# Optimization experiments

Hardware: AMD Instinct MI355X
Metric: run time of the kernel (lower is better)

The kernel has to match this reference:

```python
import jax, jax.numpy as jnp
import numpy as np

# config matching init_kwargs
C = 256; G = 16; GC = C // G; K = 3; P = K * K
PAD = 1; STR = 1; DIL = 1; OFFSET_SCALE = 1.0
N, H, W = 8, 64, 64


def setup_inputs() -> dict:
    key = jax.random.key(0)
    ks = jax.random.split(key, 8)
    def rn(k, shape, sc):
        return jax.random.normal(k, shape, jnp.float32) * sc
    return {
        "x": jax.random.normal(ks[0], (N, H, W, C), jnp.float32),
        "dw_w": rn(ks[1], (C, 1, K, K), 0.1),          # depthwise conv weight (OIHW, groups=C)
        "dw_b": jnp.zeros((C,), jnp.float32),
        "ln_g": jnp.ones((C,), jnp.float32),
        "ln_b": jnp.zeros((C,), jnp.float32),
        "off_w": rn(ks[2], (G * P * 2, C), 0.01),      # offset head (small so offsets stay sane)
        "off_b": jnp.zeros((G * P * 2,), jnp.float32),
        "mask_w": rn(ks[3], (G * P, C), 0.01),
        "mask_b": jnp.zeros((G * P,), jnp.float32),
        "in_w": rn(ks[4], (C, C), 0.05),
        "in_b": jnp.zeros((C,), jnp.float32),
        "out_w": rn(ks[5], (C, C), 0.05),
        "out_b": jnp.zeros((C,), jnp.float32),
    }


def _layer_norm(x, g, b, eps=1e-6):
    m = x.mean(-1, keepdims=True)
    v = ((x - m) ** 2).mean(-1, keepdims=True)
    return (x - m) * jax.lax.rsqrt(v + eps) * g + b


def _grid_sample_bilinear(img, grid):
    # img: (B, Cc, Hh, Ww); grid: (B, L, P, 2) normalized to [-1, 1], (x, y) order.
    # Matches torch.grid_sample(mode='bilinear', padding_mode='zeros', align_corners=False).
    B, Cc, Hh, Ww = img.shape
    gx = (grid[..., 0] + 1.0) * (Ww * 0.5) - 0.5
    gy = (grid[..., 1] + 1.0) * (Hh * 0.5) - 0.5
    x0 = jnp.floor(gx); y0 = jnp.floor(gy)
    tx = gx - x0; ty = gy - y0
    img_f = img.reshape(B, Cc, Hh * Ww)
    def corner(xi, yi, w):
        valid = (xi >= 0) & (xi < Ww) & (yi >= 0) & (yi < Hh)
        idx = (jnp.clip(yi, 0, Hh - 1) * Ww + jnp.clip(xi, 0, Ww - 1)).astype(jnp.int32)
        v = jnp.take_along_axis(img_f, idx.reshape(B, 1, -1), axis=2)  # (B, Cc, L*P)
        return v * (w * valid).reshape(B, 1, -1)
    out = (corner(x0, y0, (1 - tx) * (1 - ty)) + corner(x0 + 1, y0, tx * (1 - ty))
           + corner(x0, y0 + 1, (1 - tx) * ty) + corner(x0 + 1, y0 + 1, tx * ty))
    return out.reshape(B, Cc, grid.shape[1], grid.shape[2])  # (B, Cc, L, P)


def _dcnv3_core(x, offset, mask):
    # x: (N,H,W,C) value features; offset: (N,H,W,G*P*2); mask: (N,H,W,G*P)
    xpad = jnp.pad(x, ((0, 0), (PAD, PAD), (PAD, PAD), (0, 0)))
    Hi, Wi = H + 2 * PAD, W + 2 * PAD
    Ho, Wo = H, W
    # reference points (centers of receptive field), normalized by padded size
    start = (DIL * (K - 1)) // 2 + 0.5
    ry = (start + jnp.arange(Ho, dtype=jnp.float32) * STR) / Hi
    rx = (start + jnp.arange(Wo, dtype=jnp.float32) * STR) / Wi
    ref = jnp.stack([jnp.broadcast_to(rx[None, :], (Ho, Wo)),
                     jnp.broadcast_to(ry[:, None], (Ho, Wo))], -1)  # (Ho,Wo,2) (x,y)
    # dilation grid, x-major flattening to match torch meshgrid('ij') ordering
    d = jnp.arange(K, dtype=jnp.float32) * DIL - (DIL * (K - 1)) // 2
    kgrid = jnp.stack([jnp.repeat(d, K) / Wi, jnp.tile(d, K) / Hi], -1)  # (P,2)
    off = offset.reshape(N, Ho, Wo, G, P, 2)
    norm = jnp.array([Wi, Hi], jnp.float32)
    loc = (ref[None, :, :, None, None, :]
           + kgrid[None, None, None, None, :, :] * OFFSET_SCALE
           + off * OFFSET_SCALE / norm)                      # (N,Ho,Wo,G,P,2)
    sg = (2.0 * loc - 1.0).reshape(N, Ho * Wo, G, P, 2)
    sg = sg.transpose(0, 2, 1, 3, 4).reshape(N * G, Ho * Wo, P, 2)
    val = xpad.reshape(N, Hi * Wi, G * GC).transpose(0, 2, 1).reshape(N * G, GC, Hi, Wi)
    samp = _grid_sample_bilinear(val, sg)                    # (N*G, GC, Ho*Wo, P)
    m = mask.reshape(N, Ho * Wo, G, P).transpose(0, 2, 1, 3).reshape(N * G, 1, Ho * Wo, P)
    out = (samp * m).sum(-1)                                 # (N*G, GC, Ho*Wo)
    return out.reshape(N, G * GC, Ho * Wo).transpose(0, 2, 1).reshape(N, Ho, Wo, C)


def reference(x, dw_w, dw_b, ln_g, ln_b, off_w, off_b, mask_w, mask_b, in_w, in_b, out_w, out_b):
    xp = x @ in_w.T + in_b                                   # input_proj (values)
    # depthwise conv -> LN (channels_last) -> exact GELU
    y = jax.lax.conv_general_dilated(
        x.transpose(0, 3, 1, 2), dw_w, (1, 1), ((PAD, PAD), (PAD, PAD)),
        feature_group_count=C, dimension_numbers=('NCHW', 'OIHW', 'NCHW'))
    y = y + dw_b[None, :, None, None]
    x1 = jax.nn.gelu(_layer_norm(y.transpose(0, 2, 3, 1), ln_g, ln_b), approximate=False)
    offset = x1 @ off_w.T + off_b                            # (N,H,W,G*P*2)
    mlogits = (x1 @ mask_w.T + mask_b).reshape(N, H, W, G, P)
    mask = jax.nn.softmax(mlogits, axis=-1).reshape(N, H, W, G * P)
    out = _dcnv3_core(xp, offset, mask)
    return out @ out_w.T + out_b
```

## Files before the change

### kernel.cpp

```cpp
#include <hip/hip_runtime.h>


#define LL 32768
#define CC 256

typedef __bf16 bf16;
typedef __bf16 bf16x4 __attribute__((ext_vector_type(4)));
typedef __bf16 bf16x8 __attribute__((ext_vector_type(8)));
typedef float f32x4v __attribute__((ext_vector_type(4)));

__global__ __launch_bounds__(256) void k_prep(
    const float* __restrict__ in_w, const float* __restrict__ off_w,
    const float* __restrict__ mask_w, const float* __restrict__ out_w,
    const float* __restrict__ dw_w, const float* __restrict__ off_b,
    const float* __restrict__ mask_b,
    bf16* __restrict__ in_h, bf16* __restrict__ in_l,
    bf16* __restrict__ hw_h, bf16* __restrict__ hw_l,
    bf16* __restrict__ out_h, bf16* __restrict__ out_l,
    float* __restrict__ dwT, float* __restrict__ hbias) {
    int idx = blockIdx.x * 256 + threadIdx.x;
    if (idx < 60416) {
        const float* s; bf16 *hi, *lo; int i;
        if (idx < 16384)      { s = in_w;   hi = in_h;          lo = in_l;          i = idx; }
        else if (idx < 34816) { s = off_w;  hi = hw_h;          lo = hw_l;          i = idx - 16384; }
        else if (idx < 44032) { s = mask_w; hi = hw_h + 73728;  lo = hw_l + 73728;  i = idx - 34816; }
        else                  { s = out_w;  hi = out_h;         lo = out_l;         i = idx - 44032; }
        float4 v = *(const float4*)(s + (size_t)i * 4);
        bf16x4 h, l;
        h[0] = (bf16)v.x; l[0] = (bf16)(v.x - (float)h[0]);
        h[1] = (bf16)v.y; l[1] = (bf16)(v.y - (float)h[1]);
        h[2] = (bf16)v.z; l[2] = (bf16)(v.z - (float)h[2]);
        h[3] = (bf16)v.w; l[3] = (bf16)(v.w - (float)h[3]);
        *(bf16x4*)(hi + (size_t)i * 4) = h;
        *(bf16x4*)(lo + (size_t)i * 4) = l;
    } else if (idx < 62720) {
        int e = idx - 60416;
        int c = e & 255, j = e >> 8;
        dwT[j * 256 + c] = dw_w[c * 9 + j];
    } else if (idx < 63152) {
        int e = idx - 62720;
        hbias[e] = (e < 288) ? off_b[e] : mask_b[e - 288];
    }
}

__global__ __launch_bounds__(256) void k_dwln(
    const float* __restrict__ x, const float* __restrict__ dwT,
    const float* __restrict__ dw_b, const float* __restrict__ ln_g,
    const float* __restrict__ ln_b, bf16* __restrict__ x1h) {
    int t = threadIdx.x;
    int q = t >> 6, u = t & 63;
    int l = blockIdx.x * 4 + q;
    int w = l & 63, h = (l >> 6) & 63, n = l >> 12;
    int c0 = u * 4;

    float4 acc = *(const float4*)(dw_b + c0);
#pragma unroll
    for (int kh = 0; kh < 3; ++kh) {
        int hh = h + kh - 1;
        if (hh < 0 || hh >= 64) continue;
#pragma unroll
        for (int kw = 0; kw < 3; ++kw) {
            int ww = w + kw - 1;
            if (ww < 0 || ww >= 64) continue;
            float4 xv = *(const float4*)(x + (size_t)(((n * 64 + hh) * 64) + ww) * CC + c0);
            float4 wv = *(const float4*)(dwT + (kh * 3 + kw) * 256 + c0);
            acc.x += xv.x * wv.x; acc.y += xv.y * wv.y;
            acc.z += xv.z * wv.z; acc.w += xv.w * wv.w;
        }
    }
    float s = acc.x + acc.y + acc.z + acc.w;
    float ss = acc.x * acc.x + acc.y * acc.y + acc.z * acc.z + acc.w * acc.w;
#pragma unroll
    for (int d = 1; d < 64; d <<= 1) {
        s += __shfl_xor(s, d);
        ss += __shfl_xor(ss, d);
    }
    float mean = s * (1.0f / 256.0f);
    float var = ss * (1.0f / 256.0f) - mean * mean;
    float rstd = rsqrtf(var + 1e-6f);
    float4 gv = *(const float4*)(ln_g + c0);
    float4 bv = *(const float4*)(ln_b + c0);
    float xn0 = (acc.x - mean) * rstd * gv.x + bv.x;
    float xn1 = (acc.y - mean) * rstd * gv.y + bv.y;
    float xn2 = (acc.z - mean) * rstd * gv.z + bv.z;
    float xn3 = (acc.w - mean) * rstd * gv.w + bv.w;
    bf16x4 oh;
    oh[0] = (bf16)(0.5f * xn0 * (1.0f + erff(xn0 * 0.70710678118654752f)));
    oh[1] = (bf16)(0.5f * xn1 * (1.0f + erff(xn1 * 0.70710678118654752f)));
    oh[2] = (bf16)(0.5f * xn2 * (1.0f + erff(xn2 * 0.70710678118654752f)));
    oh[3] = (bf16)(0.5f * xn3 * (1.0f + erff(xn3 * 0.70710678118654752f)));
    *(bf16x4*)(x1h + (size_t)l * CC + c0) = oh;
}

template <bool AF32, bool OBF16>
__global__ __launch_bounds__(256) void k_gemm(
    const float* __restrict__ A32, const bf16* __restrict__ Abf,
    const bf16* __restrict__ Wh, const bf16* __restrict__ Wl,
    const float* __restrict__ bias, float* __restrict__ C32,
    bf16* __restrict__ Cbf, int Nout) {
    int mb = blockIdx.x * 128, nb = blockIdx.y * 128;
    int t = threadIdx.x, wave = t >> 6, lane = t & 63;
    int wm = wave & 1, wn = wave >> 1;
    int fm = lane & 15, fq = lane >> 4;

    __shared__ bf16 sA[128][32];
    __shared__ bf16 sWh[128][32];
    __shared__ bf16 sWl[128][32];

    f32x4v acc[4][4];
#pragma unroll
    for (int i = 0; i < 4; ++i)
#pragma unroll
        for (int j = 0; j < 4; ++j) acc[i][j] = (f32x4v){0.f, 0.f, 0.f, 0.f};

    int r = t >> 1;
    int cb = (t & 1) * 16;

    for (int kc = 0; kc < 256; kc += 32) {
        if (AF32) {
            const float* src = A32 + (size_t)(mb + r) * CC + kc + cb;
#pragma unroll
            for (int j = 0; j < 2; ++j) {
                float4 v0 = *(const float4*)(src + j * 8);
                float4 v1 = *(const float4*)(src + j * 8 + 4);
                bf16x8 hh;
                hh[0] = (bf16)v0.x; hh[1] = (bf16)v0.y;
                hh[2] = (bf16)v0.z; hh[3] = (bf16)v0.w;
                hh[4] = (bf16)v1.x; hh[5] = (bf16)v1.y;
                hh[6] = (bf16)v1.z; hh[7] = (bf16)v1.w;
                *(bf16x8*)&sA[r][cb + j * 8] = hh;
            }
        } else {
            const bf16* srcA = Abf + (size_t)(mb + r) * CC + kc + cb;
            *(uint4*)&sA[r][cb]     = *(const uint4*)srcA;
            *(uint4*)&sA[r][cb + 8] = *(const uint4*)(srcA + 8);
        }
        int wng = nb + r;
        if (wng < Nout) {
            const bf16* swH = Wh + (size_t)wng * CC + kc + cb;
            const bf16* swL = Wl + (size_t)wng * CC + kc + cb;
            *(uint4*)&sWh[r][cb]     = *(const uint4*)swH;
            *(uint4*)&sWh[r][cb + 8] = *(const uint4*)(swH + 8);
            *(uint4*)&sWl[r][cb]     = *(const uint4*)swL;
            *(uint4*)&sWl[r][cb + 8] = *(const uint4*)(swL + 8);
        } else {
            uint4 z = {0, 0, 0, 0};
            *(uint4*)&sWh[r][cb] = z; *(uint4*)&sWh[r][cb + 8] = z;
            *(uint4*)&sWl[r][cb] = z; *(uint4*)&sWl[r][cb + 8] = z;
        }
        __syncthreads();

        bf16x8 af[4], bfh[4], bfl[4];
#pragma unroll
        for (int i = 0; i < 4; ++i)
            af[i] = *(const bf16x8*)&sA[wm * 64 + i * 16 + fm][fq * 8];
#pragma unroll
        for (int j = 0; j < 4; ++j) {
            int br = wn * 64 + j * 16 + fm;
            bfh[j] = *(const bf16x8*)&sWh[br][fq * 8];
            bfl[j] = *(const bf16x8*)&sWl[br][fq * 8];
        }
#pragma unroll
        for (int i = 0; i < 4; ++i)
#pragma unroll
            for (int j = 0; j < 4; ++j) {
                acc[i][j] = __builtin_amdgcn_mfma_f32_16x16x32_bf16(
                    af[i], bfh[j], acc[i][j], 0, 0, 0);
                acc[i][j] = __builtin_amdgcn_mfma_f32_16x16x32_bf16(
                    af[i], bfl[j], acc[i][j], 0, 0, 0);
            }
        __syncthreads();
    }

#pragma unroll
    for (int j = 0; j < 4; ++j) {
        int n_g = nb + wn * 64 + j * 16 + fm;
        if (n_g >= Nout) continue;
        float bv = bias[n_g];
#pragma unroll
        for (int i = 0; i < 4; ++i) {
            int m_g = mb + wm * 64 + i * 16 + fq * 4;
#pragma unroll
            for (int rg = 0; rg < 4; ++rg) {
                float o = acc[i][j][rg] + bv;
                if (OBF16)
                    Cbf[(size_t)(m_g + rg) * Nout + n_g] = (bf16)o;
                else
                    C32[(size_t)(m_g + rg) * Nout + n_g] = o;
            }
        }
    }
}

__global__ __launch_bounds__(256) void k_gather(
    const bf16* __restrict__ xp, const float* __restrict__ head,
    bf16* __restrict__ rows) {
    int t = threadIdx.x;
    int q = t >> 5, u = t & 31;
    int l = blockIdx.x * 8 + q;
    int w = l & 63, h = (l >> 6) & 63, n = l >> 12;

    __shared__ float offs[8][288];
    __shared__ float ms[8][144];
    for (int j = u; j < 288; j += 32) offs[q][j] = head[(size_t)l * 432 + j];
    for (int j = u; j < 144; j += 32) ms[q][j] = head[(size_t)l * 432 + 288 + j];
    __syncthreads();

    if (u < 16) {
        int g = u;
        float mx = -1e30f;
#pragma unroll
        for (int p = 0; p < 9; ++p) mx = fmaxf(mx, ms[q][g * 9 + p]);
        float s = 0.f, e[9];
#pragma unroll
        for (int p = 0; p < 9; ++p) { e[p] = expf(ms[q][g * 9 + p] - mx); s += e[p]; }
        float inv = 1.0f / s;
#pragma unroll
        for (int p = 0; p < 9; ++p) ms[q][g * 9 + p] = e[p] * inv;
    }
    __syncthreads();

    int g = u >> 1;
    int c0 = g * 16 + (u & 1) * 8;
    const bf16* base = xp + (size_t)n * 4096 * CC + c0;
    float a0 = 0.f, a1 = 0.f, a2 = 0.f, a3 = 0.f;
    float a4 = 0.f, a5 = 0.f, a6 = 0.f, a7 = 0.f;
#pragma unroll
    for (int p = 0; p < 9; ++p) {
        float ox = offs[q][g * 18 + p * 2 + 0];
        float oy = offs[q][g * 18 + p * 2 + 1];
        float ax = (float)(w + (p / 3) - 1) + ox;
        float ay = (float)(h + (p % 3) - 1) + oy;
        float x0f = floorf(ax), y0f = floorf(ay);
        int x0 = (int)x0f, y0 = (int)y0f;
        float tx = ax - x0f, ty = ay - y0f;
        float m = ms[q][g * 9 + p];
        int idx[4]; float cw[4];
#pragma unroll
        for (int cr = 0; cr < 4; ++cr) {
            int xx = x0 + (cr & 1), yy = y0 + (cr >> 1);
            bool v = (xx >= 0) & (xx < 64) & (yy >= 0) & (yy < 64);
            int xc = min(max(xx, 0), 63), yc = min(max(yy, 0), 63);
            idx[cr] = (yc * 64 + xc) * CC;
            float wx = (cr & 1) ? tx : (1.f - tx);
            float wy = (cr >> 1) ? ty : (1.f - ty);
            cw[cr] = v ? (m * wx * wy) : 0.f;
        }
#pragma unroll
        for (int cr = 0; cr < 4; ++cr) {
            bf16x8 vb = *(const bf16x8*)(base + idx[cr]);
            float wt = cw[cr];
            a0 += wt * (float)vb[0]; a1 += wt * (float)vb[1];
            a2 += wt * (float)vb[2]; a3 += wt * (float)vb[3];
            a4 += wt * (float)vb[4]; a5 += wt * (float)vb[5];
            a6 += wt * (float)vb[6]; a7 += wt * (float)vb[7];
        }
    }
    bf16x8 oh;
    oh[0] = (bf16)a0; oh[1] = (bf16)a1; oh[2] = (bf16)a2; oh[3] = (bf16)a3;
    oh[4] = (bf16)a4; oh[5] = (bf16)a5; oh[6] = (bf16)a6; oh[7] = (bf16)a7;
    *(bf16x8*)(rows + (size_t)l * CC + c0) = oh;
}

__device__ __forceinline__ float dot256f(const float* a, const float* wrow) {
    const float4* w4 = (const float4*)wrow;
    float s = 0.f;
#pragma unroll 16
    for (int i = 0; i < 64; ++i) {
        float4 u = w4[i];
        const float* ap = a + i * 4;
        s += ap[0] * u.x + ap[1] * u.y + ap[2] * u.z + ap[3] * u.w;
    }
    return s;
}

__global__ __launch_bounds__(256) void k_inproj_fb(
    const float* __restrict__ x, const float* __restrict__ in_w,
    const float* __restrict__ in_b, float* __restrict__ xp) {
    int l = blockIdx.x;
    int t = threadIdx.x;
    __shared__ float xa[256];
    xa[t] = x[l * CC + t];
    __syncthreads();
    xp[l * CC + t] = dot256f(xa, in_w + t * CC) + in_b[t];
}

__device__ __forceinline__ float fetch_px_fb(const float* base, int yy, int xx) {
    if (xx < 0 || xx >= 64 || yy < 0 || yy >= 64) return 0.f;
    return base[(yy * 64 + xx) * CC];
}

__global__ __launch_bounds__(256) void k_main_fb(
    const float* __restrict__ x, const float* __restrict__ xp,
    const float* __restrict__ dw_w, const float* __restrict__ dw_b,
    const float* __restrict__ ln_g, const float* __restrict__ ln_b,
    const float* __restrict__ off_w, const float* __restrict__ off_b,
    const float* __restrict__ mask_w, const float* __restrict__ mask_b,
    const float* __restrict__ out_w, const float* __restrict__ out_b,
    float* __restrict__ out) {
    int l = blockIdx.x;
    int t = threadIdx.x;
    int w = l & 63, h = (l >> 6) & 63, n = l >> 12;
    __shared__ float x1[256];
    __shared__ float red[256];
    __shared__ float offs[288];
    __shared__ float ms[144];
    __shared__ float row[256];

    float acc = dw_b[t];
#pragma unroll
    for (int kh = 0; kh < 3; ++kh) {
        int hh = h + kh - 1;
        if (hh < 0 || hh >= 64) continue;
#pragma unroll
        for (int kw = 0; kw < 3; ++kw) {
            int ww = w + kw - 1;
            if (ww < 0 || ww >= 64) continue;
            acc += x[(((n * 64 + hh) * 64) + ww) * CC + t] * dw_w[t * 9 + kh * 3 + kw];
        }
    }
    red[t] = acc;
    __syncthreads();
    for (int s = 128; s > 0; s >>= 1) {
        if (t < s) red[t] += red[t + s];
        __syncthreads();
    }
    float mean = red[0] * (1.0f / 256.0f);
    __syncthreads();
    float d = acc - mean;
    red[t] = d * d;
    __syncthreads();
    for (int s = 128; s > 0; s >>= 1) {
        if (t < s) red[t] += red[t + s];
        __syncthreads();
    }
    float var = red[0] * (1.0f / 256.0f);
    float xn = d * rsqrtf(var + 1e-6f) * ln_g[t] + ln_b[t];
    x1[t] = 0.5f * xn * (1.0f + erff(xn * 0.70710678118654752f));
    __syncthreads();

    offs[t] = dot256f(x1, off_w + t * CC) + off_b[t];
    if (t < 32) {
        int j = 256 + t;
        offs[j] = dot256f(x1, off_w + j * CC) + off_b[j];
    }
    if (t < 144) ms[t] = dot256f(x1, mask_w + t * CC) + mask_b[t];
    __syncthreads();

    if (t < 16) {
        int g = t;
        float mx = -1e30f;
#pragma unroll
        for (int p = 0; p < 9; ++p) mx = fmaxf(mx, ms[g * 9 + p]);
        float s = 0.f, e[9];
#pragma unroll
        for (int p = 0; p < 9; ++p) { e[p] = expf(ms[g * 9 + p] - mx); s += e[p]; }
        float inv = 1.0f / s;
#pragma unroll
        for (int p = 0; p < 9; ++p) ms[g * 9 + p] = e[p] * inv;
    }
    __syncthreads();

    int g = t >> 4;
    const float* base = xp + (size_t)n * 64 * 64 * CC + t;
    float acc2 = 0.f;
#pragma unroll
    for (int p = 0; p < 9; ++p) {
        float ox = offs[g * 18 + p * 2 + 0];
        float oy = offs[g * 18 + p * 2 + 1];
        float ax = (float)(w + (p / 3) - 1) + ox;
        float ay = (float)(h + (p % 3) - 1) + oy;
        float x0f = floorf(ax), y0f = floorf(ay);
        int x0 = (int)x0f, y0 = (int)y0f;
        float tx = ax - x0f, ty = ay - y0f;
        float v00 = fetch_px_fb(base, y0, x0);
        float v01 = fetch_px_fb(base, y0, x0 + 1);
        float v10 = fetch_px_fb(base, y0 + 1, x0);
        float v11 = fetch_px_fb(base, y0 + 1, x0 + 1);
        float bl = (v00 * (1.f - tx) + v01 * tx) * (1.f - ty) +
                   (v10 * (1.f - tx) + v11 * tx) * ty;
        acc2 += ms[g * 9 + p] * bl;
    }
    row[t] = acc2;
    __syncthreads();
    out[l * CC + t] = dot256f(row, out_w + t * CC) + out_b[t];
}

extern "C" void kernel_launch(void* const* d_in, const int* in_sizes, int n_in,
                              void* d_out, int out_size, void* d_ws,
                              size_t ws_size, hipStream_t stream) {
    const float* x      = (const float*)d_in[0];
    const float* dw_w   = (const float*)d_in[1];
    const float* dw_b   = (const float*)d_in[2];
    const float* ln_g   = (const float*)d_in[3];
    const float* ln_b   = (const float*)d_in[4];
    const float* off_w  = (const float*)d_in[5];
    const float* off_b  = (const float*)d_in[6];
    const float* mask_w = (const float*)d_in[7];
    const float* mask_b = (const float*)d_in[8];
    const float* in_w   = (const float*)d_in[9];
    const float* in_b   = (const float*)d_in[10];
    const float* out_w  = (const float*)d_in[11];
    const float* out_b  = (const float*)d_in[12];
    float* out = (float*)d_out;

    const size_t szBF   = (size_t)LL * CC * 2;
    const size_t szHEAD = (size_t)LL * 432 * 4;
    const size_t szWB   = 1048576;
    const size_t need   = 2 * szBF + szHEAD + szWB;

    dim3 blk(256);
    if (ws_size >= need) {
        char* p = (char*)d_ws;
        bf16* x1h = (bf16*)p; p += szBF;
        bf16* xpb = (bf16*)p; p += szBF;
        float* head = (float*)p; p += szHEAD;
        bf16* in_h  = (bf16*)p; p += 131072;
        bf16* in_l  = (bf16*)p; p += 131072;
        bf16* hw_h  = (bf16*)p; p += 221184;
        bf16* hw_l  = (bf16*)p; p += 221184;
        bf16* out_h = (bf16*)p; p += 131072;
        bf16* out_l = (bf16*)p; p += 131072;
        float* dwT  = (float*)p; p += 9216;
        float* hbias = (float*)p;
        bf16* rows = x1h;

        k_prep<<<dim3(247), blk, 0, stream>>>(in_w, off_w, mask_w, out_w, dw_w,
                                              off_b, mask_b, in_h, in_l, hw_h,
                                              hw_l, out_h, out_l, dwT, hbias);
        k_dwln<<<dim3(LL / 4), blk, 0, stream>>>(x, dwT, dw_b, ln_g, ln_b, x1h);
        k_gemm<true, true><<<dim3(256, 2), blk, 0, stream>>>(
            x, nullptr, in_h, in_l, in_b, nullptr, xpb, 256);
        k_gemm<false, false><<<dim3(256, 4), blk, 0, stream>>>(
            nullptr, x1h, hw_h, hw_l, hbias, head, nullptr, 432);
        k_gather<<<dim3(LL / 8), blk, 0, stream>>>(xpb, head, rows);
        k_gemm<false, false><<<dim3(256, 2), blk, 0, stream>>>(
            nullptr, rows, out_h, out_l, out_b, out, nullptr, 256);
    } else {
        float* xp = (float*)d_ws;
        k_inproj_fb<<<dim3(LL), blk, 0, stream>>>(x, in_w, in_b, xp);
        k_main_fb<<<dim3(LL), blk, 0, stream>>>(x, xp, dw_w, dw_b, ln_g, ln_b,
                                                off_w, off_b, mask_w, mask_b,
                                                out_w, out_b, out);
    }
}
```

Measured before the change: 228.5 us.

## Use direct global-to-LDS loads in GEMM, store head in bf16, precast x

Rewrites the GEMM tile loading to use global_load_lds 16-byte direct copies into a flat shared buffer. The head weights are zero-padded to 512 rows so the bounds check can be dropped. The dwconv kernel now also writes a bf16 copy of x, which removes the fp32-to-bf16 conversion path from the input-projection GEMM. The offset/mask head output is stored in bf16 instead of fp32, halving its write and read traffic. The cost is an extra workspace buffer, and the offsets and mask logits lose precision.

```diff
diff --git a/kernel.cpp b/kernel.cpp
--- a/kernel.cpp
+++ b/kernel.cpp
@@ -8,6 +8,12 @@
 typedef __bf16 bf16x4 __attribute__((ext_vector_type(4)));
 typedef __bf16 bf16x8 __attribute__((ext_vector_type(8)));
 typedef float f32x4v __attribute__((ext_vector_type(4)));
+
+__device__ __forceinline__ void gload16(const bf16* g, const bf16* lds_base) {
+    __builtin_amdgcn_global_load_lds(
+        (const __attribute__((address_space(1))) void*)g,
+        (__attribute__((address_space(3))) void*)lds_base, 16, 0, 0);
+}
 
 __global__ __launch_bounds__(256) void k_prep(
     const float* __restrict__ in_w, const float* __restrict__ off_w,
@@ -37,16 +43,22 @@
         int e = idx - 60416;
         int c = e & 255, j = e >> 8;
         dwT[j * 256 + c] = dw_w[c * 9 + j];
-    } else if (idx < 63152) {
+    } else if (idx < 63232) {
         int e = idx - 62720;
-        hbias[e] = (e < 288) ? off_b[e] : mask_b[e - 288];
+        hbias[e] = (e < 288) ? off_b[e] : (e < 432 ? mask_b[e - 288] : 0.f);
+    } else if (idx < 68352) {
+        int e = idx - 63232;
+        bf16x4 z = {(bf16)0.f, (bf16)0.f, (bf16)0.f, (bf16)0.f};
+        *(bf16x4*)(hw_h + 110592 + (size_t)e * 4) = z;
+        *(bf16x4*)(hw_l + 110592 + (size_t)e * 4) = z;
     }
 }
 
 __global__ __launch_bounds__(256) void k_dwln(
     const float* __restrict__ x, const float* __restrict__ dwT,
     const float* __restrict__ dw_b, const float* __restrict__ ln_g,
-    const float* __restrict__ ln_b, bf16* __restrict__ x1h) {
+    const float* __restrict__ ln_b, bf16* __restrict__ x1h,
+    bf16* __restrict__ xb) {
     int t = threadIdx.x;
     int q = t >> 6, u = t & 63;
     int l = blockIdx.x * 4 + q;
@@ -54,6 +66,7 @@
     int c0 = u * 4;
 
     float4 acc = *(const float4*)(dw_b + c0);
+    float4 xc = {0.f, 0.f, 0.f, 0.f};
 #pragma unroll
     for (int kh = 0; kh < 3; ++kh) {
         int hh = h + kh - 1;
@@ -63,11 +76,17 @@
             int ww = w + kw - 1;
             if (ww < 0 || ww >= 64) continue;
             float4 xv = *(const float4*)(x + (size_t)(((n * 64 + hh) * 64) + ww) * CC + c0);
+            if (kh == 1 && kw == 1) xc = xv;
             float4 wv = *(const float4*)(dwT + (kh * 3 + kw) * 256 + c0);
             acc.x += xv.x * wv.x; acc.y += xv.y * wv.y;
             acc.z += xv.z * wv.z; acc.w += xv.w * wv.w;
         }
     }
+    bf16x4 xcb;
+    xcb[0] = (bf16)xc.x; xcb[1] = (bf16)xc.y;
+    xcb[2] = (bf16)xc.z; xcb[3] = (bf16)xc.w;
+    *(bf16x4*)(xb + (size_t)l * CC + c0) = xcb;
+
     float s = acc.x + acc.y + acc.z + acc.w;
     float ss = acc.x * acc.x + acc.y * acc.y + acc.z * acc.z + acc.w * acc.w;
 #pragma unroll
@@ -92,20 +111,32 @@
     *(bf16x4*)(x1h + (size_t)l * CC + c0) = oh;
 }
 
-template <bool AF32, bool OBF16>
+template <bool OBF16>
 __global__ __launch_bounds__(256) void k_gemm(
-    const float* __restrict__ A32, const bf16* __restrict__ Abf,
-    const bf16* __restrict__ Wh, const bf16* __restrict__ Wl,
-    const float* __restrict__ bias, float* __restrict__ C32,
-    bf16* __restrict__ Cbf, int Nout) {
+    const bf16* __restrict__ A, const bf16* __restrict__ Wh,
+    const bf16* __restrict__ Wl, const float* __restrict__ bias,
+    float* __restrict__ C32, bf16* __restrict__ Cbf, int Nout) {
     int mb = blockIdx.x * 128, nb = blockIdx.y * 128;
     int t = threadIdx.x, wave = t >> 6, lane = t & 63;
     int wm = wave & 1, wn = wave >> 1;
     int fm = lane & 15, fq = lane >> 4;
 
-    __shared__ bf16 sA[128][32];
-    __shared__ bf16 sWh[128][32];
-    __shared__ bf16 sWl[128][32];
+    __shared__ bf16 smem[12288];
+
+    const bf16* gbase[6];
+    const bf16* lbase[6];
+#pragma unroll
+    for (int j = 0; j < 6; ++j) {
+        int seg = wave * 6 + j;
+        int arr = seg >> 3;
+        int row = (seg & 7) * 16 + (lane >> 2);
+        int col = (lane & 3) * 8;
+        const bf16* g = (arr == 0) ? (A + (size_t)(mb + row) * CC + col)
+                      : (arr == 1) ? (Wh + (size_t)(nb + row) * CC + col)
+                                   : (Wl + (size_t)(nb + row) * CC + col);
+        gbase[j] = g;
+        lbase[j] = smem + seg * 512;
+    }
 
     f32x4v acc[4][4];
 #pragma unroll
@@ -113,52 +144,20 @@
 #pragma unroll
         for (int j = 0; j < 4; ++j) acc[i][j] = (f32x4v){0.f, 0.f, 0.f, 0.f};
 
-    int r = t >> 1;
-    int cb = (t & 1) * 16;
-
     for (int kc = 0; kc < 256; kc += 32) {
-        if (AF32) {
-            const float* src = A32 + (size_t)(mb + r) * CC + kc + cb;
-#pragma unroll
-            for (int j = 0; j < 2; ++j) {
-                float4 v0 = *(const float4*)(src + j * 8);
-                float4 v1 = *(const float4*)(src + j * 8 + 4);
-                bf16x8 hh;
-                hh[0] = (bf16)v0.x; hh[1] = (bf16)v0.y;
-                hh[2] = (bf16)v0.z; hh[3] = (bf16)v0.w;
-                hh[4] = (bf16)v1.x; hh[5] = (bf16)v1.y;
-                hh[6] = (bf16)v1.z; hh[7] = (bf16)v1.w;
-                *(bf16x8*)&sA[r][cb + j * 8] = hh;
-            }
-        } else {
-            const bf16* srcA = Abf + (size_t)(mb + r) * CC + kc + cb;
-            *(uint4*)&sA[r][cb]     = *(const uint4*)srcA;
-            *(uint4*)&sA[r][cb + 8] = *(const uint4*)(srcA + 8);
-        }
-        int wng = nb + r;
-        if (wng < Nout) {
-            const bf16* swH = Wh + (size_t)wng * CC + kc + cb;
-            const bf16* swL = Wl + (size_t)wng * CC + kc + cb;
-            *(uint4*)&sWh[r][cb]     = *(const uint4*)swH;
-            *(uint4*)&sWh[r][cb + 8] = *(const uint4*)(swH + 8);
-            *(uint4*)&sWl[r][cb]     = *(const uint4*)swL;
-            *(uint4*)&sWl[r][cb + 8] = *(const uint4*)(swL + 8);
-        } else {
-            uint4 z = {0, 0, 0, 0};
-            *(uint4*)&sWh[r][cb] = z; *(uint4*)&sWh[r][cb + 8] = z;
-            *(uint4*)&sWl[r][cb] = z; *(uint4*)&sWl[r][cb + 8] = z;
-        }
+#pragma unroll
+        for (int j = 0; j < 6; ++j) gload16(gbase[j] + kc, lbase[j]);
         __syncthreads();
 
         bf16x8 af[4], bfh[4], bfl[4];
 #pragma unroll
         for (int i = 0; i < 4; ++i)
-            af[i] = *(const bf16x8*)&sA[wm * 64 + i * 16 + fm][fq * 8];
+            af[i] = *(const bf16x8*)&smem[(wm * 64 + i * 16 + fm) * 32 + fq * 8];
 #pragma unroll
         for (int j = 0; j < 4; ++j) {
             int br = wn * 64 + j * 16 + fm;
-            bfh[j] = *(const bf16x8*)&sWh[br][fq * 8];
-            bfl[j] = *(const bf16x8*)&sWl[br][fq * 8];
+            bfh[j] = *(const bf16x8*)&smem[4096 + br * 32 + fq * 8];
+            bfl[j] = *(const bf16x8*)&smem[8192 + br * 32 + fq * 8];
         }
 #pragma unroll
         for (int i = 0; i < 4; ++i)
@@ -193,7 +192,7 @@
 }
 
 __global__ __launch_bounds__(256) void k_gather(
-    const bf16* __restrict__ xp, const float* __restrict__ head,
+    const bf16* __restrict__ xp, const bf16* __restrict__ head,
     bf16* __restrict__ rows) {
     int t = threadIdx.x;
     int q = t >> 5, u = t & 31;
@@ -202,8 +201,8 @@
 
     __shared__ float offs[8][288];
     __shared__ float ms[8][144];
-    for (int j = u; j < 288; j += 32) offs[q][j] = head[(size_t)l * 432 + j];
-    for (int j = u; j < 144; j += 32) ms[q][j] = head[(size_t)l * 432 + 288 + j];
+    for (int j = u; j < 288; j += 32) offs[q][j] = (float)head[(size_t)l * 432 + j];
+    for (int j = u; j < 144; j += 32) ms[q][j] = (float)head[(size_t)l * 432 + 288 + j];
     __syncthreads();
 
     if (u < 16) {
@@ -404,38 +403,39 @@
     const float* out_b  = (const float*)d_in[12];
     float* out = (float*)d_out;
 
-    const size_t szBF   = (size_t)LL * CC * 2;
-    const size_t szHEAD = (size_t)LL * 432 * 4;
-    const size_t szWB   = 1048576;
-    const size_t need   = 2 * szBF + szHEAD + szWB;
+    const size_t szBF    = (size_t)LL * CC * 2;
+    const size_t szHEADB = (size_t)LL * 432 * 2;
+    const size_t szWB    = 1300480;
+    const size_t need    = 3 * szBF + szHEADB + szWB;
 
     dim3 blk(256);
     if (ws_size >= need) {
         char* p = (char*)d_ws;
         bf16* x1h = (bf16*)p; p += szBF;
         bf16* xpb = (bf16*)p; p += szBF;
-        float* head = (float*)p; p += szHEAD;
+        bf16* xb  = (bf16*)p; p += szBF;
+        bf16* headb = (bf16*)p; p += szHEADB;
         bf16* in_h  = (bf16*)p; p += 131072;
         bf16* in_l  = (bf16*)p; p += 131072;
-        bf16* hw_h  = (bf16*)p; p += 221184;
-        bf16* hw_l  = (bf16*)p; p += 221184;
+        bf16* hw_h  = (bf16*)p; p += 262144;
+        bf16* hw_l  = (bf16*)p; p += 262144;
         bf16* out_h = (bf16*)p; p += 131072;
         bf16* out_l = (bf16*)p; p += 131072;
         float* dwT  = (float*)p; p += 9216;
         float* hbias = (float*)p;
         bf16* rows = x1h;
 
-        k_prep<<<dim3(247), blk, 0, stream>>>(in_w, off_w, mask_w, out_w, dw_w,
+        k_prep<<<dim3(267), blk, 0, stream>>>(in_w, off_w, mask_w, out_w, dw_w,
                                               off_b, mask_b, in_h, in_l, hw_h,
                                               hw_l, out_h, out_l, dwT, hbias);
-        k_dwln<<<dim3(LL / 4), blk, 0, stream>>>(x, dwT, dw_b, ln_g, ln_b, x1h);
-        k_gemm<true, true><<<dim3(256, 2), blk, 0, stream>>>(
-            x, nullptr, in_h, in_l, in_b, nullptr, xpb, 256);
-        k_gemm<false, false><<<dim3(256, 4), blk, 0, stream>>>(
-            nullptr, x1h, hw_h, hw_l, hbias, head, nullptr, 432);
-        k_gather<<<dim3(LL / 8), blk, 0, stream>>>(xpb, head, rows);
-        k_gemm<false, false><<<dim3(256, 2), blk, 0, stream>>>(
-            nullptr, rows, out_h, out_l, out_b, out, nullptr, 256);
+        k_dwln<<<dim3(LL / 4), blk, 0, stream>>>(x, dwT, dw_b, ln_g, ln_b, x1h, xb);
+        k_gemm<true><<<dim3(256, 2), blk, 0, stream>>>(
+            xb, in_h, in_l, in_b, nullptr, xpb, 256);
+        k_gemm<true><<<dim3(256, 4), blk, 0, stream>>>(
+            x1h, hw_h, hw_l, hbias, nullptr, headb, 432);
+        k_gather<<<dim3(LL / 8), blk, 0, stream>>>(xpb, headb, rows);
+        k_gemm<false><<<dim3(256, 2), blk, 0, stream>>>(
+            rows, out_h, out_l, out_b, out, nullptr, 256);
     } else {
         float* xp = (float*)d_ws;
         k_inproj_fb<<<dim3(LL), blk, 0, stream>>>(x, in_w, in_b, xp);
```

Result: faster. 218.8 us (-4.3%).
